# Kernel tuning notes

Hardware: AMD Instinct MI355X
Metric: run time of the kernel (lower is better)

Reference implementation:

```python
import jax, jax.numpy as jnp
import numpy as np

B, C, N, D, K, M, E, G = 2, 64, 16384, 3, 128, 1, 262144, 3


def setup_inputs() -> dict:
    key = jax.random.key(0)
    ks = jax.random.split(key, 15)
    scale = 1.0 / (C * C)
    return {
        "x": jax.random.normal(ks[0], (B, C, N), jnp.float32),
        "nodes": jax.random.uniform(ks[1], (B, N, D), jnp.float32),
        "node_weights": jax.random.uniform(ks[2], (B, N, M), jnp.float32),
        "geo": jax.random.normal(ks[3], (B, G, N), jnp.float32),
        "directed_edges": jax.random.randint(ks[4], (B, E, 2), 0, N, jnp.int32),
        "edge_gradient_weights": 0.1 * jax.random.normal(ks[5], (B, E, D), jnp.float32),
        "modes": jax.random.normal(ks[6], (K, D, M), jnp.float32),
        "weights_c": scale * jax.random.uniform(ks[7], (C, C, K, M), jnp.float32),
        "weights_s": scale * jax.random.uniform(ks[8], (C, C, K, M), jnp.float32),
        "weights_0": scale * jax.random.uniform(ks[9], (C, C, 1, M), jnp.float32),
        "W": jax.random.normal(ks[10], (C, C), jnp.float32) / np.sqrt(C),
        "gw": jax.random.normal(ks[11], (C, C * D), jnp.float32) / np.sqrt(C * D),
        "geo_wx": jax.random.normal(ks[12], (C, G), jnp.float32) / np.sqrt(G),
        "wx": jax.random.normal(ks[13], (C, C), jnp.float32) / np.sqrt(C),
        "w2": jax.random.normal(ks[14], (C, C), jnp.float32) / np.sqrt(C),
    }


def reference(x, nodes, node_weights, geo, directed_edges, edge_gradient_weights,
              modes, weights_c, weights_s, weights_0, W, gw, geo_wx, wx, w2):
    # ---- Fourier bases: cos(kx), sin(kx), 1 -------------------------------
    temp = jnp.einsum('bxd,kdw->bxkw', nodes, modes)          # [B,N,K,M]
    bases_c, bases_s = jnp.cos(temp), jnp.sin(temp)
    b, n = temp.shape[0], temp.shape[1]
    bases_0 = jnp.ones((b, n, 1, temp.shape[3]), temp.dtype)
    nw = node_weights[:, :, None, :]                          # quadrature weights
    wb_c, wb_s, wb_0 = bases_c * nw, bases_s * nw, bases_0 * nw

    # ---- Spectral convolution (non-uniform Fourier neural layer) ----------
    x_c = jnp.einsum('bix,bxkw->bikw', x, wb_c)
    x_s = -jnp.einsum('bix,bxkw->bikw', x, wb_s)
    x_0 = jnp.einsum('bix,bxkw->bikw', x, wb_0)
    f_c = jnp.einsum('bikw,iokw->bokw', x_c, weights_c) - jnp.einsum('bikw,iokw->bokw', x_s, weights_s)
    f_s = jnp.einsum('bikw,iokw->bokw', x_s, weights_c) + jnp.einsum('bikw,iokw->bokw', x_c, weights_s)
    f_0 = jnp.einsum('bikw,iokw->bokw', x_0, weights_0)
    x1 = (jnp.einsum('bokw,bxkw->box', f_0, bases_0)
          + 2.0 * jnp.einsum('bokw,bxkw->box', f_c, bases_c)
          - 2.0 * jnp.einsum('bokw,bxkw->box', f_s, bases_s))

    # ---- Pointwise linear W ----------------------------------------------
    x2 = jnp.einsum('oi,bix->box', W, x)

    # ---- Least-squares gradient via edge gather + scatter-add -------------
    fT = jnp.transpose(x, (0, 2, 1))                          # [B,N,C]
    tgt, src = directed_edges[..., 0], directed_edges[..., 1]  # [B,E]
    f_src = jnp.take_along_axis(fT, src[:, :, None], axis=1)   # [B,E,C]
    f_tgt = jnp.take_along_axis(fT, tgt[:, :, None], axis=1)
    df = f_src - f_tgt
    # message[b,e,c,d] = w[b,e,d] * df[b,e,c], flattened c-major -> [B,E,C*D]
    msg = (df[..., :, None] * edge_gradient_weights[..., None, :]).reshape(b, tgt.shape[1], -1)
    gradf = jnp.zeros((b, n, msg.shape[-1]), msg.dtype).at[jnp.arange(b)[:, None], tgt].add(msg)
    x3 = jnp.einsum('og,bng->bon', gw, gradf)                  # [B,C,N]

    # ---- Geo embedding: w2 @ (softsign(geo_wx@geo) * (wx@x)) --------------
    h = jax.nn.soft_sign(jnp.einsum('og,bgx->box', geo_wx, geo)) * jnp.einsum('oi,bix->box', wx, x)
    x4 = jnp.einsum('oi,bix->box', w2, h)

    return jax.nn.gelu(x1 + x2 + x3 + x4, approximate=False)
```

## Files before the change

kernel.cpp:

```cpp
#include <hip/hip_runtime.h>
#include <hip/hip_fp16.h>
#include <math.h>

#define BB 2
#define CC 64
#define NN 16384
#define DD 3
#define KK 128
#define EE 262144
#define GG 3
#define PP 128
#define PP2 64
#define LL (NN/PP)
#define KTOT 576

typedef short bf16x8 __attribute__((ext_vector_type(8)));
typedef float f32x4  __attribute__((ext_vector_type(4)));

__device__ __forceinline__ short f2bf(float f) {
    unsigned u = __float_as_uint(f);
    u += 0x7FFF + ((u >> 16) & 1);
    return (short)(u >> 16);
}
__device__ __forceinline__ float bf2f(unsigned short u) {
    return __uint_as_float(((unsigned)u) << 16);
}

constexpr size_t OFF_XB   = 0;
constexpr size_t OFF_PC   = OFF_XB   + (size_t)BB*NN*32;
constexpr size_t OFF_PS   = OFF_PC   + (size_t)BB*PP*CC*KK;
constexpr size_t OFF_BIN4 = OFF_PC;
constexpr size_t OFF_AC   = OFF_PS   + (size_t)BB*PP*CC*KK;
constexpr size_t OFF_AS   = OFF_AC   + (size_t)BB*CC*KK;
constexpr size_t OFF_F0   = OFF_AS   + (size_t)BB*CC*KK;
constexpr size_t OFF_X0   = OFF_F0   + (size_t)BB*CC;
constexpr size_t OFF_CNT  = OFF_X0   + (size_t)BB*CC;
constexpr size_t OFF_OFFS = OFF_CNT  + (size_t)BB*NN;
constexpr size_t OFF_RANK = OFF_OFFS + (size_t)BB*NN;
constexpr size_t OFF_GRB  = OFF_RANK + (size_t)BB*EE;
constexpr size_t OFF_APAN = OFF_GRB  + (size_t)BB*NN*96;
constexpr size_t OFF_GWXT = OFF_APAN + (size_t)BB*KTOT*CC/2;

#define S_A0 (BB*(NN/64))
#define S_A1 (S_A0 + BB*CC)
#define S_A2 (S_A1 + (BB*EE)/256)
#define S_A3 (S_A2 + 48)
#define S_A4 (S_A3 + BB*PP2*4)
__global__ void __launch_bounds__(256) k1(const float* __restrict__ x,
                                          const float* __restrict__ nwt,
                                          const int* __restrict__ edges,
                                          const float* __restrict__ W,
                                          const float* __restrict__ gw,
                                          const float* __restrict__ geo_wx,
                                          const float* __restrict__ w2,
                                          const float* __restrict__ nodes,
                                          const float* __restrict__ modes,
                                          unsigned short* __restrict__ xB,
                                          float* __restrict__ x0,
                                          int* __restrict__ counts,
                                          int* __restrict__ rank,
                                          float* __restrict__ gwxT,
                                          short* __restrict__ ApanB,
                                          float* __restrict__ pc,
                                          float* __restrict__ ps) {
    int blk = blockIdx.x;
    int tid = threadIdx.x;
    __shared__ __align__(16) char smem[36864];
    if (blk < S_A0) {
        float (*tile)[65] = (float (*)[65])smem;
        int b = blk / (NN/64);
        int n0 = (blk % (NN/64)) * 64;
        int c = tid & 63, r4 = tid >> 6;
        for (int rr = 0; rr < 16; rr++) {
            int i = r4*16 + rr;
            tile[i][c] = x[((size_t)b*CC + i)*NN + n0 + c];
        }
        __syncthreads();
        for (int rr = 0; rr < 16; rr++) {
            int nn = r4*16 + rr;
            xB[((size_t)b*NN + n0 + nn)*64 + c] = (unsigned short)f2bf(tile[c][nn]);
        }
    } else if (blk < S_A1) {
        float* red = (float*)smem;
        int bi = blk - S_A0;
        int b = bi >> 6, i = bi & 63;
        const float4* __restrict__ xr = (const float4*)&x[((size_t)b*CC + i)*NN];
        const float4* __restrict__ wr = (const float4*)&nwt[(size_t)b*NN];
        float s = 0.f;
        for (int t = tid; t < NN/4; t += 256) {
            float4 xv = xr[t];
            float4 wv = wr[t];
            s += xv.x*wv.x + xv.y*wv.y + xv.z*wv.z + xv.w*wv.w;
        }
        red[tid] = s;
        __syncthreads();
        for (int off = 128; off > 0; off >>= 1) {
            if (tid < off) red[tid] += red[tid+off];
            __syncthreads();
        }
        if (tid == 0) x0[b*CC + i] = red[0];
    } else if (blk < S_A2) {
        int idx = (blk - S_A1)*256 + tid;
        int tgt = edges[(size_t)idx*2 + 0];
        int b = idx / EE;
        rank[idx] = atomicAdd(&counts[b*NN + tgt], 1);
    } else if (blk < S_A3) {
        int idx = (blk - S_A2)*256 + tid;
        if (idx < CC*CC) {
            int j = idx>>6, o = idx&63;
            short wv  = f2bf(W[o*CC+j]);
            short w2v = f2bf(w2[o*CC+j]);
            ApanB[((size_t)(0*CC+o))*KTOT + 256 + j] = wv;
            ApanB[((size_t)(1*CC+o))*KTOT + 256 + j] = wv;
            ApanB[((size_t)(0*CC+o))*KTOT + 320 + j] = w2v;
            ApanB[((size_t)(1*CC+o))*KTOT + 320 + j] = w2v;
        }
        if (idx < CC*CC*DD) {
            int g = idx>>6, o = idx&63;
            short gv = f2bf(gw[o*(CC*DD)+g]);
            ApanB[((size_t)(0*CC+o))*KTOT + 384 + g] = gv;
            ApanB[((size_t)(1*CC+o))*KTOT + 384 + g] = gv;
        }
        if (idx < GG*CC) { int g = idx>>6, i = idx&63; gwxT[idx] = geo_wx[i*GG+g]; }
    } else {
        short* Axw = (short*)smem;
        short* Bc  = (short*)(smem + 17408);
        short* Bsn = (short*)(smem + 17408 + 8704);
        float* ndl = (float*)(smem + 17408 + 8704 + 8704);
        int bc = blk - S_A3;
        int b = bc >> 8;
        int rem = bc & 255;
        int chunk2 = rem >> 2;
        int kt = rem & 3;
        int k0 = kt * 32;
        int lane = tid & 63;
        int w = tid >> 6;
        int col = lane & 15;
        int quad = lane >> 4;
        int wk = w & 1;
        int wi = w >> 1;

        f32x4 ac[2], as4[2];
#pragma unroll
        for (int it = 0; it < 2; it++)
#pragma unroll
            for (int r = 0; r < 4; r++) { ac[it][r] = 0.f; as4[it][r] = 0.f; }

        for (int h = 0; h < 2; h++) {
            int nbase = chunk2*256 + h*128;
            if (h) __syncthreads();
            for (int e = tid; e < 128*3; e += 256) ndl[e] = nodes[((size_t)b*NN + nbase)*3 + e];
#pragma unroll
            for (int s = 0; s < 8; s++) {
                int e = tid + s*256;
                int i = e >> 5, seg = e & 31;
                float4 xv = *(const float4*)&x[((size_t)b*CC + i)*NN + nbase + seg*4];
                float4 wv = *(const float4*)&nwt[(size_t)b*NN + nbase + seg*4];
                unsigned lo = (unsigned)(unsigned short)f2bf(xv.x*wv.x)
                            | ((unsigned)(unsigned short)f2bf(xv.y*wv.y) << 16);
                unsigned hi = (unsigned)(unsigned short)f2bf(xv.z*wv.z)
                            | ((unsigned)(unsigned short)f2bf(xv.w*wv.w) << 16);
                *(uint2*)&Axw[i*136 + seg*4] = make_uint2(lo, hi);
            }
            __syncthreads();
#pragma unroll
            for (int s = 0; s < 16; s++) {
                int e = tid + s*256;
                int n = e & 127, kl = e >> 7;
                int k = k0 + kl;
                float t = ndl[n*3+0]*modes[k*3+0] + ndl[n*3+1]*modes[k*3+1]
                        + ndl[n*3+2]*modes[k*3+2];
                Bc [kl*136 + n] = f2bf(__cosf(t));
                Bsn[kl*136 + n] = f2bf(__sinf(t));
            }
            __syncthreads();

            int rowB = (wk*16 + col)*136;
#pragma unroll
            for (int ns = 0; ns < 4; ns++) {
                int koff = ns*32 + quad*8;
                bf16x8 bcf = *(bf16x8*)&Bc [rowB + koff];
                bf16x8 bsf = *(bf16x8*)&Bsn[rowB + koff];
#pragma unroll
                for (int it = 0; it < 2; it++) {
                    int itile = wi*2 + it;
                    bf16x8 af = *(bf16x8*)&Axw[(itile*16 + col)*136 + koff];
                    ac[it]  = __builtin_amdgcn_mfma_f32_16x16x32_bf16(af, bcf, ac[it], 0, 0, 0);
                    as4[it] = __builtin_amdgcn_mfma_f32_16x16x32_bf16(af, bsf, as4[it], 0, 0, 0);
                }
            }
        }
        int base = (b*PP2 + chunk2)*CC;
        int kw = k0 + wk*16 + col;
#pragma unroll
        for (int it = 0; it < 2; it++) {
#pragma unroll
            for (int r = 0; r < 4; r++) {
                int i = (wi*2 + it)*16 + quad*4 + r;
                pc[(size_t)(base + i)*KK + kw] = ac[it][r];
                ps[(size_t)(base + i)*KK + kw] = as4[it][r];
            }
        }
    }
}

__global__ void __launch_bounds__(256) k2(const float* __restrict__ pc, const float* __restrict__ ps,
                                          float* __restrict__ Ac, float* __restrict__ As,
                                          const int* __restrict__ counts,
                                          int* __restrict__ offsets) {
    int blk = blockIdx.x;
    int tid = threadIdx.x;
    if (blk < 256) {
        int idx = blk*64 + (tid >> 2);
        int sub = tid & 3;
        if (idx >= BB*CC*KK) return;
        int b = idx / (CC*KK);
        int r = idx % (CC*KK);
        float sc = 0.f, ss = 0.f;
        for (int ch = sub; ch < PP2; ch += 4) {
            size_t o = ((size_t)(b*PP2 + ch)*CC)*KK + r;
            sc += pc[o]; ss += ps[o];
        }
        sc += __shfl_xor(sc, 1); sc += __shfl_xor(sc, 2);
        ss += __shfl_xor(ss, 1); ss += __shfl_xor(ss, 2);
        if (sub == 0) { Ac[idx] = sc; As[idx] = ss; }
    } else {
        int b = blk - 256;
        __shared__ int part[256];
        int base = b*NN + tid*64;
        int s = 0;
        for (int j = 0; j < 64; j++) s += counts[base + j];
        part[tid] = s;
        __syncthreads();
        for (int off = 1; off < 256; off <<= 1) {
            int v = (tid >= off) ? part[tid - off] : 0;
            __syncthreads();
            part[tid] += v;
            __syncthreads();
        }
        int excl = part[tid] - s;
        for (int j = 0; j < 64; j++) {
            int c = counts[base + j];
            offsets[base + j] = excl;
            excl += c;
        }
    }
}

__global__ void __launch_bounds__(256) k3(const float* __restrict__ Ac, const float* __restrict__ As_,
                                          const float* __restrict__ wc, const float* __restrict__ wsw,
                                          const float* __restrict__ w0, const float* __restrict__ x0,
                                          const int* __restrict__ edges, const float* __restrict__ egw,
                                          const int* __restrict__ offs, const int* __restrict__ rank,
                                          float4* __restrict__ bin4,
                                          short* __restrict__ ApanB, float* __restrict__ f0) {
    int idx = blockIdx.x;
    int tid = threadIdx.x;
    if (idx >= BB*CC*2) {
        int e = (idx - BB*CC*2)*256 + tid;
        int b = e / EE;
        int tgt = edges[(size_t)e*2+0];
        int src = edges[(size_t)e*2+1];
        const float* __restrict__ ew = &egw[(size_t)e*3];
        float e0 = ew[0], e1 = ew[1], e2 = ew[2];
        int pos = offs[b*NN+tgt] + rank[e];
        bin4[(size_t)b*EE + pos] = make_float4(__int_as_float(src), e0, e1, e2);
        return;
    }
    int b = idx / (CC*2);
    int rem = idx % (CC*2);
    int o = rem >> 1, khalf = rem & 1;
    int kl = tid & 63, ig = tid >> 6;
    int k = khalf*64 + kl;
    float fc = 0.f, fs = 0.f;
    for (int ii = 0; ii < 16; ii++) {
        int i = ig*16 + ii;
        float a_c = Ac[(b*CC+i)*KK + k];
        float a_s = As_[(b*CC+i)*KK + k];
        float wcc = wc[((size_t)(i*CC+o))*KK + k];
        float wss = wsw[((size_t)(i*CC+o))*KK + k];
        fc += a_c*wcc + a_s*wss;
        fs += a_c*wss - a_s*wcc;
    }
    __shared__ float rc[256], rs[256];
    __shared__ float f0s[64];
    rc[tid] = fc; rs[tid] = fs;
    if (khalf == 0 && tid < 64) f0s[tid] = x0[b*CC + tid] * w0[tid*CC + o];
    __syncthreads();
    if (ig == 0) {
        fc = rc[kl] + rc[64+kl] + rc[128+kl] + rc[192+kl];
        fs = rs[kl] + rs[64+kl] + rs[128+kl] + rs[192+kl];
        unsigned pk = (unsigned)(unsigned short)f2bf(2.f*fc)
                    | ((unsigned)(unsigned short)f2bf(-2.f*fs) << 16);
        ((unsigned*)ApanB)[((size_t)(b*CC + o))*(KTOT/2) + k] = pk;
    }
    if (khalf == 0 && tid == 0) {
        float acc = 0.f;
        for (int i = 0; i < 64; i++) acc += f0s[i];
        f0[b*CC+o] = acc;
    }
}

__global__ void __launch_bounds__(512, 8) k_eg(const unsigned short* __restrict__ xB,
                                               const int* __restrict__ offsets,
                                               const float4* __restrict__ bin4,
                                               const float* __restrict__ nodes,
                                               const float* __restrict__ modes,
                                               const float* __restrict__ geo,
                                               const short* __restrict__ ApanB,
                                               const float* __restrict__ f0,
                                               const float* __restrict__ wx,
                                               const float* __restrict__ gwxT,
                                               float* __restrict__ out) {
    int blk = blockIdx.x;
    int b  = blk >> 9;
    int n0 = (blk & 511) * 32;
    int tid = threadIdx.x;
    int lane = tid & 63;
    int w = tid >> 6;
    int wr = w >> 1;
    int wc = w & 1;
    int col  = lane & 15;
    int quad = lane >> 4;
    int quad8 = quad * 8;
    int quad4 = quad * 4;

    __shared__ __align__(16) char smem[37776];
    short* As = (short*)smem;
    short* Bs = (short*)(smem + 9216);
    short* Ws = (short*)(smem + 13824);
    unsigned short* gradfL = (unsigned short*)(smem + 23040);
    float* ndl  = (float*)(smem + 36864);
    float* geo3 = (float*)(smem + 37248);
    int* soff   = (int*)(smem + 37632);

    if (tid < 96) ndl[tid]  = nodes[((size_t)b*NN + n0)*3 + tid];
    if (tid < 96) geo3[tid] = geo[((size_t)b*GG + (tid >> 5))*NN + n0 + (tid & 31)];
    if (tid >= 128 && tid < 161) {
        int idx = n0 + tid - 128;
        soff[tid - 128] = (idx < NN) ? offsets[b*NN + idx] : EE;
    }
    for (int e = tid; e < 4096; e += 512) {
        int i = e >> 6, j = e & 63;
        Ws[i*72 + j] = f2bf(wx[i*64 + j]);
    }
    f32x4 acc, xwa;
#pragma unroll
    for (int r = 0; r < 4; r++) { acc[r] = f0[b*CC + wr*16 + quad4 + r]; xwa[r] = 0.f; }
    __syncthreads();

    const unsigned short* __restrict__ xBb = xB + (size_t)b*NN*64 + lane;
    const float4* __restrict__ binb = bin4 + (size_t)b*EE;
    for (int q = 0; q < 4; q++) {
        int nl = w*4 + q;
        int js = soff[nl], je = soff[nl+1];
        float a0 = 0.f, a1 = 0.f, a2 = 0.f, s0 = 0.f, s1 = 0.f, s2 = 0.f;
#pragma unroll 4
        for (int j = js; j < je; j++) {
            float4 e = binb[j];
            int src = __float_as_int(e.x);
            float xs = bf2f(xBb[(size_t)src*64]);
            a0 = fmaf(xs, e.y, a0);
            a1 = fmaf(xs, e.z, a1);
            a2 = fmaf(xs, e.w, a2);
            s0 += e.y; s1 += e.z; s2 += e.w;
        }
        float xtgt = bf2f(xBb[(size_t)(n0 + nl)*64]);
        float fv0 = a0 - xtgt*s0;
        float fv1 = a1 - xtgt*s1;
        float fv2 = a2 - xtgt*s2;
        int g0 = lane*3;
        gradfL[(g0>>6)*2304 + nl*72 + (g0&63)] = (unsigned short)f2bf(fv0);
        int g1 = g0 + 1;
        gradfL[(g1>>6)*2304 + nl*72 + (g1&63)] = (unsigned short)f2bf(fv1);
        int g2 = g0 + 2;
        gradfL[(g2>>6)*2304 + nl*72 + (g2&63)] = (unsigned short)f2bf(fv2);
    }

    const short* __restrict__ Ab = ApanB + ((size_t)b*CC)*KTOT;

    for (int c = 0; c < 9; c++) {
        __syncthreads();
        {
            int o = tid >> 3, seg = tid & 7;
            *(uint4*)&As[o*72 + seg*8] =
                *(const uint4*)&Ab[(size_t)o*KTOT + c*64 + seg*8];
        }
        if (c < 4) {
#pragma unroll
            for (int s = 0; s < 2; s++) {
                int e = tid + s*512;
                int n = e >> 5, kpl = e & 31;
                int kp = c*32 + kpl;
                float t = ndl[n*3+0]*modes[kp*3+0] + ndl[n*3+1]*modes[kp*3+1]
                        + ndl[n*3+2]*modes[kp*3+2];
                unsigned pk = (unsigned)(unsigned short)f2bf(__cosf(t))
                            | ((unsigned)(unsigned short)f2bf(__sinf(t)) << 16);
                ((unsigned*)Bs)[n*36 + kpl] = pk;
            }
        } else if (c == 4) {
            if (tid < 256) {
                int n = tid >> 3, seg = tid & 7;
                *(uint4*)&Bs[n*72 + seg*8] =
                    *(const uint4*)&xB[((size_t)(b*NN + n0 + n))*64 + seg*8];
            }
        } else if (c == 5) {
            int n = wc*16 + col;
            float gv0 = geo3[n], gv1 = geo3[32+n], gv2 = geo3[64+n];
#pragma unroll
            for (int r = 0; r < 4; r++) {
                int i = wr*16 + quad4 + r;
                float t = gwxT[i]*gv0 + gwxT[64+i]*gv1 + gwxT[128+i]*gv2;
                float ssv = t / (1.f + fabsf(t));
                Bs[n*72 + i] = f2bf(ssv * xwa[r]);
            }
        }
        __syncthreads();
        const short* Bbase = (c >= 6) ? (const short*)&gradfL[(size_t)(c-6)*2304] : Bs;
        int rowA = (wr*16 + col) * 72;
        int rowB = (wc*16 + col) * 72;
#pragma unroll
        for (int ko = 0; ko < 2; ko++) {
            int koff = ko*32 + quad8;
            bf16x8 af = *(bf16x8*)&As[rowA + koff];
            bf16x8 bfv = *(bf16x8*)&Bbase[rowB + koff];
            acc = __builtin_amdgcn_mfma_f32_16x16x32_bf16(af, bfv, acc, 0, 0, 0);
            if (c == 4) {
                bf16x8 wf = *(bf16x8*)&Ws[rowA + koff];
                xwa = __builtin_amdgcn_mfma_f32_16x16x32_bf16(wf, bfv, xwa, 0, 0, 0);
            }
        }
    }
#pragma unroll
    for (int r = 0; r < 4; r++) {
        int o = wr*16 + quad4 + r;
        float v = acc[r];
        float g = 0.5f * v * (1.f + erff(v * 0.70710678118654752f));
        out[((size_t)b*CC + o)*NN + n0 + wc*16 + col] = g;
    }
}

extern "C" void kernel_launch(void* const* d_in, const int* in_sizes, int n_in,
                              void* d_out, int out_size, void* d_ws, size_t ws_size,
                              hipStream_t stream) {
    const float* x      = (const float*)d_in[0];
    const float* nodes  = (const float*)d_in[1];
    const float* nwt    = (const float*)d_in[2];
    const float* geo    = (const float*)d_in[3];
    const int*   edges  = (const int*)d_in[4];
    const float* egw    = (const float*)d_in[5];
    const float* modes  = (const float*)d_in[6];
    const float* wc     = (const float*)d_in[7];
    const float* wsw    = (const float*)d_in[8];
    const float* w0     = (const float*)d_in[9];
    const float* W      = (const float*)d_in[10];
    const float* gw     = (const float*)d_in[11];
    const float* geo_wx = (const float*)d_in[12];
    const float* wx     = (const float*)d_in[13];
    const float* w2     = (const float*)d_in[14];

    float* ws   = (float*)d_ws;
    unsigned short* xB  = (unsigned short*)(ws + OFF_XB);
    float* pc   = ws + OFF_PC;
    float* ps   = ws + OFF_PS;
    float* Ac   = ws + OFF_AC;
    float* As_  = ws + OFF_AS;
    float* f0   = ws + OFF_F0;
    float* x0   = ws + OFF_X0;
    int*  counts = (int*)(ws + OFF_CNT);
    int*  offs   = (int*)(ws + OFF_OFFS);
    int*  rank   = (int*)(ws + OFF_RANK);
    float4* bin4 = (float4*)(ws + OFF_BIN4);
    short* ApanB  = (short*)(ws + OFF_APAN);
    float* gwxT   = ws + OFF_GWXT;
    float* out  = (float*)d_out;

    hipMemsetAsync(counts, 0, (size_t)(BB*NN)*sizeof(int), stream);

    k1 <<<S_A4, 256, 0, stream>>>(x, nwt, edges, W, gw, geo_wx, w2, nodes, modes,
                                  xB, x0, counts, rank, gwxT, ApanB, pc, ps);
    k2 <<<256 + BB, 256, 0, stream>>>(pc, ps, Ac, As_, counts, offs);
    k3 <<<BB*CC*2 + (BB*EE)/256, 256, 0, stream>>>(Ac, As_, wc, wsw, w0, x0,
                                                   edges, egw, offs, rank, bin4, ApanB, f0);
    k_eg <<<BB*(NN/32), 512, 0, stream>>>(xB, offs, bin4, nodes, modes, geo,
                                          ApanB, f0, wx, gwxT, out);
}
```

Before: 184.7 us.

## Fuse partial-sum reduction and offset scan into k1, drop k2

Spectral partial products are now accumulated straight into Ac/As with float atomics instead of being written to per-chunk pc/ps buffers and reduced by a separate kernel. The exclusive scan of edge counts moves into the last-finishing edge-count block of k1, detected with a done counter, so k2 is removed along with its launch and the large pc/ps workspace traffic. One memset now zeroes counts, the done flag and the accumulators. The cost is atomic contention on Ac/As, non-deterministic summation order, and a serial scan run by a single block.

```diff
diff --git a/kernel.cpp b/kernel.cpp
--- a/kernel.cpp
+++ b/kernel.cpp
@@ -9,9 +9,7 @@
 #define KK 128
 #define EE 262144
 #define GG 3
-#define PP 128
 #define PP2 64
-#define LL (NN/PP)
 #define KTOT 576
 
 typedef short bf16x8 __attribute__((ext_vector_type(8)));
@@ -27,23 +25,23 @@
 }
 
 constexpr size_t OFF_XB   = 0;
-constexpr size_t OFF_PC   = OFF_XB   + (size_t)BB*NN*32;
-constexpr size_t OFF_PS   = OFF_PC   + (size_t)BB*PP*CC*KK;
-constexpr size_t OFF_BIN4 = OFF_PC;
-constexpr size_t OFF_AC   = OFF_PS   + (size_t)BB*PP*CC*KK;
+constexpr size_t OFF_CNT  = OFF_XB   + (size_t)BB*NN*32;
+constexpr size_t OFF_DONE = OFF_CNT  + (size_t)BB*NN;
+constexpr size_t OFF_AC   = OFF_DONE + 64;
 constexpr size_t OFF_AS   = OFF_AC   + (size_t)BB*CC*KK;
 constexpr size_t OFF_F0   = OFF_AS   + (size_t)BB*CC*KK;
 constexpr size_t OFF_X0   = OFF_F0   + (size_t)BB*CC;
-constexpr size_t OFF_CNT  = OFF_X0   + (size_t)BB*CC;
-constexpr size_t OFF_OFFS = OFF_CNT  + (size_t)BB*NN;
+constexpr size_t OFF_OFFS = OFF_X0   + (size_t)BB*CC;
 constexpr size_t OFF_RANK = OFF_OFFS + (size_t)BB*NN;
-constexpr size_t OFF_GRB  = OFF_RANK + (size_t)BB*EE;
-constexpr size_t OFF_APAN = OFF_GRB  + (size_t)BB*NN*96;
+constexpr size_t OFF_APAN = OFF_RANK + (size_t)BB*EE;
 constexpr size_t OFF_GWXT = OFF_APAN + (size_t)BB*KTOT*CC/2;
+constexpr size_t OFF_BIN4 = (OFF_GWXT + (size_t)GG*CC + 3) & ~(size_t)3;
+
+#define NEB ((BB*EE)/256)
 
 #define S_A0 (BB*(NN/64))
 #define S_A1 (S_A0 + BB*CC)
-#define S_A2 (S_A1 + (BB*EE)/256)
+#define S_A2 (S_A1 + NEB)
 #define S_A3 (S_A2 + 48)
 #define S_A4 (S_A3 + BB*PP2*4)
 __global__ void __launch_bounds__(256) k1(const float* __restrict__ x,
@@ -61,8 +59,10 @@
                                           int* __restrict__ rank,
                                           float* __restrict__ gwxT,
                                           short* __restrict__ ApanB,
-                                          float* __restrict__ pc,
-                                          float* __restrict__ ps) {
+                                          float* __restrict__ Ac,
+                                          float* __restrict__ As,
+                                          int* __restrict__ done,
+                                          int* __restrict__ offsets) {
     int blk = blockIdx.x;
     int tid = threadIdx.x;
     __shared__ __align__(16) char smem[36864];
@@ -100,10 +100,43 @@
         }
         if (tid == 0) x0[b*CC + i] = red[0];
     } else if (blk < S_A2) {
+        int* part = (int*)smem;
+        int* flag = ((int*)smem) + 256;
         int idx = (blk - S_A1)*256 + tid;
         int tgt = edges[(size_t)idx*2 + 0];
         int b = idx / EE;
         rank[idx] = atomicAdd(&counts[b*NN + tgt], 1);
+        __syncthreads();
+        if (tid == 0) {
+            __threadfence();
+            *flag = (atomicAdd(done, 1) == NEB - 1);
+        }
+        __syncthreads();
+        if (*flag) {
+            for (int b2 = 0; b2 < BB; b2++) {
+                int base = b2*NN + tid*64;
+                int s = 0;
+                for (int j = 0; j < 64; j++)
+                    s += __hip_atomic_load(&counts[base + j], __ATOMIC_RELAXED,
+                                           __HIP_MEMORY_SCOPE_AGENT);
+                part[tid] = s;
+                __syncthreads();
+                for (int off = 1; off < 256; off <<= 1) {
+                    int v = (tid >= off) ? part[tid - off] : 0;
+                    __syncthreads();
+                    part[tid] += v;
+                    __syncthreads();
+                }
+                int excl = part[tid] - s;
+                for (int j = 0; j < 64; j++) {
+                    int c = __hip_atomic_load(&counts[base + j], __ATOMIC_RELAXED,
+                                              __HIP_MEMORY_SCOPE_AGENT);
+                    offsets[base + j] = excl;
+                    excl += c;
+                }
+                __syncthreads();
+            }
+        }
     } else if (blk < S_A3) {
         int idx = (blk - S_A2)*256 + tid;
         if (idx < CC*CC) {
@@ -190,59 +223,16 @@
                 }
             }
         }
-        int base = (b*PP2 + chunk2)*CC;
         int kw = k0 + wk*16 + col;
 #pragma unroll
         for (int it = 0; it < 2; it++) {
 #pragma unroll
             for (int r = 0; r < 4; r++) {
                 int i = (wi*2 + it)*16 + quad*4 + r;
-                pc[(size_t)(base + i)*KK + kw] = ac[it][r];
-                ps[(size_t)(base + i)*KK + kw] = as4[it][r];
-            }
-        }
-    }
-}
-
-__global__ void __launch_bounds__(256) k2(const float* __restrict__ pc, const float* __restrict__ ps,
-                                          float* __restrict__ Ac, float* __restrict__ As,
-                                          const int* __restrict__ counts,
-                                          int* __restrict__ offsets) {
-    int blk = blockIdx.x;
-    int tid = threadIdx.x;
-    if (blk < 256) {
-        int idx = blk*64 + (tid >> 2);
-        int sub = tid & 3;
-        if (idx >= BB*CC*KK) return;
-        int b = idx / (CC*KK);
-        int r = idx % (CC*KK);
-        float sc = 0.f, ss = 0.f;
-        for (int ch = sub; ch < PP2; ch += 4) {
-            size_t o = ((size_t)(b*PP2 + ch)*CC)*KK + r;
-            sc += pc[o]; ss += ps[o];
-        }
-        sc += __shfl_xor(sc, 1); sc += __shfl_xor(sc, 2);
-        ss += __shfl_xor(ss, 1); ss += __shfl_xor(ss, 2);
-        if (sub == 0) { Ac[idx] = sc; As[idx] = ss; }
-    } else {
-        int b = blk - 256;
-        __shared__ int part[256];
-        int base = b*NN + tid*64;
-        int s = 0;
-        for (int j = 0; j < 64; j++) s += counts[base + j];
-        part[tid] = s;
-        __syncthreads();
-        for (int off = 1; off < 256; off <<= 1) {
-            int v = (tid >= off) ? part[tid - off] : 0;
-            __syncthreads();
-            part[tid] += v;
-            __syncthreads();
-        }
-        int excl = part[tid] - s;
-        for (int j = 0; j < 64; j++) {
-            int c = counts[base + j];
-            offsets[base + j] = excl;
-            excl += c;
+                size_t o = (size_t)(b*CC + i)*KK + kw;
+                atomicAdd(&Ac[o], ac[it][r]);
+                atomicAdd(&As[o], as4[it][r]);
+            }
         }
     }
 }
@@ -461,27 +451,25 @@
 
     float* ws   = (float*)d_ws;
     unsigned short* xB  = (unsigned short*)(ws + OFF_XB);
-    float* pc   = ws + OFF_PC;
-    float* ps   = ws + OFF_PS;
+    int*  counts = (int*)(ws + OFF_CNT);
+    int*  done   = (int*)(ws + OFF_DONE);
     float* Ac   = ws + OFF_AC;
     float* As_  = ws + OFF_AS;
     float* f0   = ws + OFF_F0;
     float* x0   = ws + OFF_X0;
-    int*  counts = (int*)(ws + OFF_CNT);
     int*  offs   = (int*)(ws + OFF_OFFS);
     int*  rank   = (int*)(ws + OFF_RANK);
-    float4* bin4 = (float4*)(ws + OFF_BIN4);
     short* ApanB  = (short*)(ws + OFF_APAN);
     float* gwxT   = ws + OFF_GWXT;
+    float4* bin4  = (float4*)(ws + OFF_BIN4);
     float* out  = (float*)d_out;
 
-    hipMemsetAsync(counts, 0, (size_t)(BB*NN)*sizeof(int), stream);
+    hipMemsetAsync(counts, 0, (size_t)(BB*NN + 64 + 2*BB*CC*KK)*sizeof(float), stream);
 
     k1 <<<S_A4, 256, 0, stream>>>(x, nwt, edges, W, gw, geo_wx, w2, nodes, modes,
-                                  xB, x0, counts, rank, gwxT, ApanB, pc, ps);
-    k2 <<<256 + BB, 256, 0, stream>>>(pc, ps, Ac, As_, counts, offs);
-    k3 <<<BB*CC*2 + (BB*EE)/256, 256, 0, stream>>>(Ac, As_, wc, wsw, w0, x0,
-                                                   edges, egw, offs, rank, bin4, ApanB, f0);
+                                  xB, x0, counts, rank, gwxT, ApanB, Ac, As_, done, offs);
+    k3 <<<BB*CC*2 + NEB, 256, 0, stream>>>(Ac, As_, wc, wsw, w0, x0,
+                                           edges, egw, offs, rank, bin4, ApanB, f0);
     k_eg <<<BB*(NN/32), 512, 0, stream>>>(xB, offs, bin4, nodes, modes, geo,
                                           ApanB, f0, wx, gwxT, out);
 }
```

After: 265.1 us. +43.6%, slower.
